# Kernel optimization log

Hardware: AMD Instinct MI355X
Metric: run time of the kernel (lower is better)

Reference implementation:

```python
import jax, jax.numpy as jnp
import numpy as np

N, NF, D, H, L, FFN, E, EF = 2048, 64, 256, 8, 6, 1024, 32768, 16
HD = D // H
MAXDEG, MAXDIST = 64, 8


def setup_inputs() -> dict:
    key = jax.random.key(0)
    ks = jax.random.split(key, 32)
    s = 0.02
    nrm = lambda k, sh: (jax.random.normal(k, sh, jnp.float32) * s)
    return {
        "x": jax.random.normal(ks[0], (N, NF), jnp.float32),
        "edge_attr": jax.random.normal(ks[1], (E, EF), jnp.float32),
        "node_proj_w": nrm(ks[2], (D, NF)),
        "node_proj_b": jnp.zeros((D,), jnp.float32),
        "in_deg_emb": nrm(ks[3], (MAXDEG + 1, D)),
        "out_deg_emb": nrm(ks[4], (MAXDEG + 1, D)),
        "dist_bias": nrm(ks[5], (MAXDIST + 2, H)),
        "edge_proj_w": nrm(ks[6], (H, EF)),
        "edge_proj_b": jnp.zeros((H,), jnp.float32),
        "cls_token": nrm(ks[7], (1, D)),
        "q_w": nrm(ks[8], (L, D, D)), "q_b": jnp.zeros((L, D)),
        "k_w": nrm(ks[9], (L, D, D)), "k_b": jnp.zeros((L, D)),
        "v_w": nrm(ks[10], (L, D, D)), "v_b": jnp.zeros((L, D)),
        "o_w": nrm(ks[11], (L, D, D)), "o_b": jnp.zeros((L, D)),
        "ffn1_w": nrm(ks[12], (L, FFN, D)), "ffn1_b": jnp.zeros((L, FFN)),
        "ffn2_w": nrm(ks[13], (L, D, FFN)), "ffn2_b": jnp.zeros((L, D)),
        "ln1_s": jnp.ones((L, D)), "ln1_b": jnp.zeros((L, D)),
        "ln2_s": jnp.ones((L, D)), "ln2_b": jnp.zeros((L, D)),
        "fn_s": jnp.ones((D,)), "fn_b": jnp.zeros((D,)),
        "edge_index": jax.random.randint(ks[14], (2, E), 0, N, dtype=jnp.int32),
        "dist_matrix": jax.random.randint(ks[15], (N, N), 0, MAXDIST + 2, dtype=jnp.int32),
    }


def _ln(v, s, b):
    m = v.mean(-1, keepdims=True)
    va = v.var(-1, keepdims=True)
    return (v - m) / jnp.sqrt(va + 1e-5) * s + b


def _forward(x, edge_attr, node_proj_w, node_proj_b, in_deg_emb, out_deg_emb,
             dist_bias, edge_proj_w, edge_proj_b, cls_token,
             q_w, q_b, k_w, k_b, v_w, v_b, o_w, o_b,
             ffn1_w, ffn1_b, ffn2_w, ffn2_b,
             ln1_s, ln1_b, ln2_s, ln2_b, fn_s, fn_b,
             edge_index, dist_matrix):
    # node embedding + degree encoding
    h = x @ node_proj_w.T + node_proj_b  # (N, D)
    ones = jnp.ones((E,), jnp.int32)
    in_deg = jnp.clip(jax.ops.segment_sum(ones, edge_index[1], num_segments=N), 0, MAXDEG)
    out_deg = jnp.clip(jax.ops.segment_sum(ones, edge_index[0], num_segments=N), 0, MAXDEG)
    h = h + in_deg_emb[in_deg] + out_deg_emb[out_deg]
    h = jnp.concatenate([cls_token, h], axis=0)  # (N+1, D), CLS at row 0
    Nf = N + 1
    # spatial bias: pad dist matrix with zeros for CLS, then embed
    dist_p = jnp.pad(jnp.clip(dist_matrix, 0, MAXDIST + 1), ((1, 0), (1, 0)))
    bias = dist_bias[dist_p]  # (Nf, Nf, H)
    # edge-feature bias: scatter-add projected edge features into dense (N,N,H)
    proj = edge_attr @ edge_proj_w.T + edge_proj_b  # (E, H)
    ebias = jnp.zeros((N, N, H), h.dtype).at[edge_index[0], edge_index[1]].add(proj)
    bias = bias + jnp.pad(ebias, ((1, 0), (1, 0), (0, 0)))
    bias_t = bias.transpose(2, 0, 1)  # (H, Nf, Nf)
    scale = np.sqrt(HD).astype(np.float32)
    for l in range(L):
        hn = _ln(h, ln1_s[l], ln1_b[l])
        Q = (hn @ q_w[l].T + q_b[l]).reshape(Nf, H, HD).transpose(1, 0, 2)
        K = (hn @ k_w[l].T + k_b[l]).reshape(Nf, H, HD).transpose(1, 0, 2)
        V = (hn @ v_w[l].T + v_b[l]).reshape(Nf, H, HD).transpose(1, 0, 2)
        logits = jnp.einsum('hnd,hmd->hnm', Q, K) / scale + bias_t
        attn = jax.nn.softmax(logits, axis=-1)
        o = jnp.einsum('hnm,hmd->hnd', attn, V).transpose(1, 0, 2).reshape(Nf, D)
        h = h + o @ o_w[l].T + o_b[l]
        hn2 = _ln(h, ln2_s[l], ln2_b[l])
        h = h + jax.nn.gelu(hn2 @ ffn1_w[l].T + ffn1_b[l], approximate=False) @ ffn2_w[l].T + ffn2_b[l]
    h = _ln(h, fn_s, fn_b)
    return h, h[0]


def reference(x, edge_attr, node_proj_w, node_proj_b, in_deg_emb, out_deg_emb,
              dist_bias, edge_proj_w, edge_proj_b, cls_token,
              q_w, q_b, k_w, k_b, v_w, v_b, o_w, o_b,
              ffn1_w, ffn1_b, ffn2_w, ffn2_b,
              ln1_s, ln1_b, ln2_s, ln2_b, fn_s, fn_b,
              edge_index, dist_matrix):
    return _forward(x, edge_attr, node_proj_w, node_proj_b, in_deg_emb, out_deg_emb,
                    dist_bias, edge_proj_w, edge_proj_b, cls_token,
                    q_w, q_b, k_w, k_b, v_w, v_b, o_w, o_b,
                    ffn1_w, ffn1_b, ffn2_w, ffn2_b,
                    ln1_s, ln1_b, ln2_s, ln2_b, fn_s, fn_b,
                    edge_index, dist_matrix)
```

## Files before the change

kernel.cpp:

```cpp
#include <hip/hip_runtime.h>
#include <math.h>

#define N_ 2048
#define NF_IN 64
#define D_ 256
#define H_ 8
#define HD_ 32
#define L_ 6
#define FFN_ 1024
#define E_ 32768
#define EF_ 16
#define NF 2049
#define MAXDEG_ 64
#define BSTRIDE 2112
#define RPAD 2112
#define NSPLIT 4

typedef __attribute__((ext_vector_type(8))) short bf16x8;
typedef __attribute__((ext_vector_type(4))) float f32x4;

__device__ inline unsigned short f2b(float f){
  union { float f; unsigned u; } v; v.f = f;
  unsigned r = (v.u + 0x7fffu + ((v.u >> 16) & 1u)) >> 16;
  return (unsigned short)r;
}
__device__ inline float b2f(short s){
  union { unsigned u; float f; } v; v.u = ((unsigned)(unsigned short)s) << 16;
  return v.f;
}

__device__ inline void atomic_add_bf16(short* p, float add){
  unsigned* wp = (unsigned*)((size_t)p & ~(size_t)3);
  bool hi = ((size_t)p & 2) != 0;
  unsigned old = *wp, assumed;
  do {
    assumed = old;
    unsigned short cur = hi ? (unsigned short)(assumed >> 16)
                            : (unsigned short)(assumed & 0xffffu);
    float f = b2f((short)cur) + add;
    unsigned short nb = f2b(f);
    unsigned nw = hi ? ((assumed & 0x0000ffffu) | ((unsigned)nb << 16))
                     : ((assumed & 0xffff0000u) | (unsigned)nb);
    old = atomicCAS(wp, assumed, nw);
  } while (old != assumed);
}

__device__ inline float wred_sum(float v){
  #pragma unroll
  for (int o = 32; o > 0; o >>= 1) v += __shfl_down(v, o, 64);
  return v;
}

__global__ void zero_int(int* p, int n){
  int i = blockIdx.x * blockDim.x + threadIdx.x;
  if (i < n) p[i] = 0;
}

__global__ void deg_count(const int* __restrict__ ei, int* __restrict__ ind,
                          int* __restrict__ outd){
  int e = blockIdx.x * blockDim.x + threadIdx.x;
  if (e >= E_) return;
  atomicAdd(&outd[ei[e]], 1);
  atomicAdd(&ind[ei[E_ + e]], 1);
}

__global__ void embed_k(const float* __restrict__ x, const float* __restrict__ W,
                        const float* __restrict__ b, const float* __restrict__ inE,
                        const float* __restrict__ outE, const int* __restrict__ ind,
                        const int* __restrict__ outd, const float* __restrict__ cls,
                        float* __restrict__ h){
  int i = blockIdx.x, d = threadIdx.x;
  if (i == 0){ h[d] = cls[d]; return; }
  int n = i - 1;
  const float4* xr = (const float4*)(x + (long)n * NF_IN);
  const float4* wr = (const float4*)(W + (long)d * NF_IN);
  float acc = b[d];
  #pragma unroll
  for (int k = 0; k < NF_IN / 4; k++){
    float4 a = xr[k], w = wr[k];
    acc += a.x * w.x + a.y * w.y + a.z * w.z + a.w * w.w;
  }
  int id = min(ind[n], MAXDEG_), od = min(outd[n], MAXDEG_);
  acc += inE[(long)id * D_ + d] + outE[(long)od * D_ + d];
  h[(long)i * D_ + d] = acc;
}

__global__ void bias_fill(const int* __restrict__ dist, const float* __restrict__ db,
                          short* __restrict__ bb){
  __shared__ float lutS[10][H_];
  int i = blockIdx.x;
  if (threadIdx.x < 80) ((float*)lutS)[threadIdx.x] = db[threadIdx.x];
  __syncthreads();
  for (int u = threadIdx.x; u < BSTRIDE / 8; u += 256){
    int dp[8];
    #pragma unroll
    for (int k = 0; k < 8; k++){
      int j = u * 8 + k;
      int d = 0;
      if (i > 0 && j > 0 && j < NF){
        int dv = dist[(long)(i - 1) * N_ + (j - 1)];
        d = max(0, min(dv, 9));
      }
      dp[k] = (j < NF) ? d : -1;
    }
    #pragma unroll
    for (int h = 0; h < H_; h++){
      short s[8];
      #pragma unroll
      for (int k = 0; k < 8; k++)
        s[k] = (dp[k] >= 0) ? (short)f2b(lutS[dp[k]][h]) : (short)0;
      *(bf16x8*)(bb + ((long)h * NF + i) * BSTRIDE + u * 8) = *(bf16x8*)s;
    }
  }
}

__global__ void edge_bias(const float* __restrict__ ea, const float* __restrict__ W,
                          const float* __restrict__ b, const int* __restrict__ ei,
                          short* __restrict__ bb){
  int e = blockIdx.x * blockDim.x + threadIdx.x;
  if (e >= E_) return;
  float a[EF_];
  #pragma unroll
  for (int k = 0; k < EF_; k++) a[k] = ea[(long)e * EF_ + k];
  int src = ei[e], dst = ei[E_ + e];
  #pragma unroll
  for (int h = 0; h < H_; h++){
    float p = b[h];
    #pragma unroll
    for (int k = 0; k < EF_; k++) p += a[k] * W[h * EF_ + k];
    atomic_add_bf16(bb + ((long)h * NF + src + 1) * BSTRIDE + (dst + 1), p);
  }
}

__global__ void w2b(const float* __restrict__ src, short* __restrict__ dst,
                    long n, long per, long ostride, long ooff){
  long i = (long)blockIdx.x * 256 + threadIdx.x;
  if (i >= n) return;
  long l = i / per, r = i - l * per;
  dst[l * ostride + ooff + r] = (short)f2b(src[i]);
}

__global__ void ln_k(const float* __restrict__ in, const float* __restrict__ s,
                     const float* __restrict__ b, float* __restrict__ outf,
                     short* __restrict__ outb, int dup0){
  __shared__ float r1[4], r2[4];
  int i = blockIdx.x, d = threadIdx.x;
  float v = in[(long)i * D_ + d];
  float s1 = wred_sum(v), s2 = wred_sum(v * v);
  if ((d & 63) == 0){ r1[d >> 6] = s1; r2[d >> 6] = s2; }
  __syncthreads();
  float S1 = r1[0] + r1[1] + r1[2] + r1[3];
  float S2 = r2[0] + r2[1] + r2[2] + r2[3];
  float m = S1 * (1.0f / D_);
  float var = S2 * (1.0f / D_) - m * m;
  float y = (v - m) * rsqrtf(var + 1e-5f) * s[d] + b[d];
  if (outf){
    outf[(long)i * D_ + d] = y;
    if (dup0 && i == 0) outf[(long)NF * D_ + d] = y;
  }
  if (outb) outb[(long)i * D_ + d] = (short)f2b(y);
}

__global__ __launch_bounds__(256) void qkv_gemm(const short* __restrict__ A,
    const short* __restrict__ Wall, const float* __restrict__ qb,
    const float* __restrict__ kb, const float* __restrict__ vb,
    short* __restrict__ QKb, short* __restrict__ Vtg, int l){
  const int z = blockIdx.z;
  const short* W = Wall + ((long)(l * 3 + z)) * D_ * D_;
  const float* bsp = (z == 0) ? qb : (z == 1) ? kb : vb;
  __shared__ __align__(16) short As[64][40], Ws[64][40];
  const int tid = threadIdx.x, lane = tid & 63, wave = tid >> 6;
  const int col = lane & 15, quad = lane >> 4;
  const int wm = wave & 1, wn = wave >> 1;
  const int bm = blockIdx.x * 64, bn = blockIdx.y * 64;
  const f32x4 zero4 = {0.f, 0.f, 0.f, 0.f};
  f32x4 acc[2][2] = {{zero4, zero4}, {zero4, zero4}};
  const int row = tid >> 2, seg = tid & 3;
  for (int k0 = 0; k0 < D_; k0 += 32){
    __syncthreads();
    bf16x8 av = (bf16x8)(short)0;
    int gm = bm + row;
    if (gm < NF) av = *(const bf16x8*)(A + (long)gm * D_ + k0 + seg * 8);
    *(bf16x8*)&As[row][seg * 8] = av;
    *(bf16x8*)&Ws[row][seg * 8] = *(const bf16x8*)(W + (long)(bn + row) * D_ + k0 + seg * 8);
    __syncthreads();
    bf16x8 a0 = *(const bf16x8*)&As[wm * 32 + col][quad * 8];
    bf16x8 a1 = *(const bf16x8*)&As[wm * 32 + 16 + col][quad * 8];
    bf16x8 b0 = *(const bf16x8*)&Ws[wn * 32 + col][quad * 8];
    bf16x8 b1 = *(const bf16x8*)&Ws[wn * 32 + 16 + col][quad * 8];
    acc[0][0] = __builtin_amdgcn_mfma_f32_16x16x32_bf16(a0, b0, acc[0][0], 0, 0, 0);
    acc[0][1] = __builtin_amdgcn_mfma_f32_16x16x32_bf16(a0, b1, acc[0][1], 0, 0, 0);
    acc[1][0] = __builtin_amdgcn_mfma_f32_16x16x32_bf16(a1, b0, acc[1][0], 0, 0, 0);
    acc[1][1] = __builtin_amdgcn_mfma_f32_16x16x32_bf16(a1, b1, acc[1][1], 0, 0, 0);
  }
  #pragma unroll
  for (int i = 0; i < 2; i++)
    #pragma unroll
    for (int j = 0; j < 2; j++)
      #pragma unroll
      for (int r = 0; r < 4; r++){
        int gm = bm + wm * 32 + i * 16 + quad * 4 + r;
        if (gm >= NF) continue;
        int gn = bn + wn * 32 + j * 16 + col;
        float v = acc[i][j][r] + bsp[gn];
        if (z < 2) QKb[(long)z * NF * D_ + (long)gm * D_ + gn] = (short)f2b(v);
        else       Vtg[(long)gn * BSTRIDE + gm] = (short)f2b(v);
      }
}

template<int ACT, int RES, int OUTF, int OUTB, int ATOM>
__global__ __launch_bounds__(256) void mgemm(const short* __restrict__ A,
    const short* __restrict__ W, const float* __restrict__ bs,
    const float* __restrict__ R, float* __restrict__ Cf, short* __restrict__ Cb,
    int M, int Nn, int Kc, int Kstride){
  __shared__ __align__(16) short As[64][40], Ws[64][40];
  const int tid = threadIdx.x, lane = tid & 63, wave = tid >> 6;
  const int col = lane & 15, quad = lane >> 4;
  const int wm = wave & 1, wn = wave >> 1;
  const int bm = blockIdx.x * 64, bn = blockIdx.y * 64;
  const int koff = blockIdx.z * Kc;
  const f32x4 zero4 = {0.f, 0.f, 0.f, 0.f};
  f32x4 acc[2][2] = {{zero4, zero4}, {zero4, zero4}};
  const int row = tid >> 2, seg = tid & 3;
  for (int k0 = 0; k0 < Kc; k0 += 32){
    __syncthreads();
    bf16x8 av = (bf16x8)(short)0;
    int gm = bm + row;
    if (gm < M) av = *(const bf16x8*)(A + (long)gm * Kstride + koff + k0 + seg * 8);
    *(bf16x8*)&As[row][seg * 8] = av;
    *(bf16x8*)&Ws[row][seg * 8] =
      *(const bf16x8*)(W + (long)(bn + row) * Kstride + koff + k0 + seg * 8);
    __syncthreads();
    bf16x8 a0 = *(const bf16x8*)&As[wm * 32 + col][quad * 8];
    bf16x8 a1 = *(const bf16x8*)&As[wm * 32 + 16 + col][quad * 8];
    bf16x8 b0 = *(const bf16x8*)&Ws[wn * 32 + col][quad * 8];
    bf16x8 b1 = *(const bf16x8*)&Ws[wn * 32 + 16 + col][quad * 8];
    acc[0][0] = __builtin_amdgcn_mfma_f32_16x16x32_bf16(a0, b0, acc[0][0], 0, 0, 0);
    acc[0][1] = __builtin_amdgcn_mfma_f32_16x16x32_bf16(a0, b1, acc[0][1], 0, 0, 0);
    acc[1][0] = __builtin_amdgcn_mfma_f32_16x16x32_bf16(a1, b0, acc[1][0], 0, 0, 0);
    acc[1][1] = __builtin_amdgcn_mfma_f32_16x16x32_bf16(a1, b1, acc[1][1], 0, 0, 0);
  }
  #pragma unroll
  for (int i = 0; i < 2; i++)
    #pragma unroll
    for (int j = 0; j < 2; j++)
      #pragma unroll
      for (int r = 0; r < 4; r++){
        int gm = bm + wm * 32 + i * 16 + quad * 4 + r;
        if (gm >= M) continue;
        int gn = bn + wn * 32 + j * 16 + col;
        if (ATOM){
          float v = acc[i][j][r] + (blockIdx.z == 0 ? bs[gn] : 0.f);
          atomicAdd(&Cf[(long)gm * Nn + gn], v);
        } else {
          float v = acc[i][j][r] + bs[gn];
          if (ACT == 1) v = v * 0.5f * (1.0f + erff(v * 0.70710678118654752f));
          if (RES) v += R[(long)gm * Nn + gn];
          if (OUTF) Cf[(long)gm * Nn + gn] = v;
          if (OUTB) Cb[(long)gm * Nn + gn] = (short)f2b(v);
        }
      }
}

__global__ __launch_bounds__(256) void fattn_k(const short* __restrict__ Qb,
    const short* __restrict__ Kb, const short* __restrict__ Vtg,
    const short* __restrict__ biasb, float* __restrict__ Opart,
    float* __restrict__ Lpart){
  __shared__ __align__(16) short Ks[64][40];
  __shared__ __align__(16) short Vt[32][72];
  __shared__ __align__(16) short PB[4][16][72];

  const int tid = threadIdx.x, wave = tid >> 6, lane = tid & 63;
  const int col = lane & 15, quad = lane >> 4;
  const int h = blockIdx.y, qz = blockIdx.z;
  const int i0b = blockIdx.x * 64;
  const int i0 = i0b + wave * 16;
  const int t0 = (qz == 0) ? 0 : 9 + 8 * (qz - 1);
  const int t1 = t0 + ((qz == 0) ? 9 : 8);

  int qrow = min(i0 + col, NF - 1);
  bf16x8 qf = *(const bf16x8*)(Qb + (long)qrow * D_ + h * HD_ + quad * 8);

  f32x4 oacc0 = {0.f, 0.f, 0.f, 0.f}, oacc1 = {0.f, 0.f, 0.f, 0.f};
  float rs[4] = {0.f, 0.f, 0.f, 0.f};
  const f32x4 zero4 = {0.f, 0.f, 0.f, 0.f};
  const float scale = 0.17677669529663687f;

  for (int t = t0; t < t1; t++){
    const int j0 = t * 64;
    __syncthreads();
    {
      int key = tid >> 2, seg = tid & 3;
      int j = j0 + key;
      bf16x8 kv = (bf16x8)(short)0;
      if (j < NF) kv = *(const bf16x8*)(Kb + (long)j * D_ + h * HD_ + seg * 8);
      *(bf16x8*)&Ks[key][seg * 8] = kv;
    }
    {
      int d = tid >> 3, seg = tid & 7;
      *(bf16x8*)&Vt[d][seg * 8] =
        *(const bf16x8*)(Vtg + (long)(h * HD_ + d) * BSTRIDE + j0 + seg * 8);
    }
    #pragma unroll
    for (int it = 0; it < 2; it++){
      int idx = it * 64 + lane;
      int rw = idx >> 3, seg = idx & 7;
      int irow = min(i0b + wave * 16 + rw, NF - 1);
      *(bf16x8*)&PB[wave][rw][seg * 8] =
        *(const bf16x8*)(biasb + ((long)h * NF + irow) * BSTRIDE + j0 + seg * 8);
    }
    __syncthreads();

    f32x4 sacc[4];
    #pragma unroll
    for (int t4 = 0; t4 < 4; t4++){
      bf16x8 kf = *(const bf16x8*)&Ks[t4 * 16 + col][quad * 8];
      sacc[t4] = __builtin_amdgcn_mfma_f32_16x16x32_bf16(qf, kf, zero4, 0, 0, 0);
    }

    const bool tail = (j0 + 64 > NF);
    #pragma unroll
    for (int r = 0; r < 4; r++){
      #pragma unroll
      for (int t4 = 0; t4 < 4; t4++){
        float bv = b2f(PB[wave][quad * 4 + r][t4 * 16 + col]);
        float p = __expf(sacc[t4][r] * scale + bv);
        if (tail && (j0 + t4 * 16 + col >= NF)) p = 0.f;
        rs[r] += p;
        PB[wave][quad * 4 + r][t4 * 16 + col] = (short)f2b(p);
      }
    }

    #pragma unroll
    for (int ks = 0; ks < 2; ks++){
      bf16x8 af = *(const bf16x8*)&PB[wave][col][ks * 32 + quad * 8];
      bf16x8 v0 = *(const bf16x8*)&Vt[col][ks * 32 + quad * 8];
      bf16x8 v1 = *(const bf16x8*)&Vt[16 + col][ks * 32 + quad * 8];
      oacc0 = __builtin_amdgcn_mfma_f32_16x16x32_bf16(af, v0, oacc0, 0, 0, 0);
      oacc1 = __builtin_amdgcn_mfma_f32_16x16x32_bf16(af, v1, oacc1, 0, 0, 0);
    }
  }

  #pragma unroll
  for (int r = 0; r < 4; r++){
    #pragma unroll
    for (int o = 1; o < 16; o <<= 1) rs[r] += __shfl_xor(rs[r], o, 64);
  }
  long pi = ((long)qz * H_ + h) * RPAD + i0 + quad * 4;
  #pragma unroll
  for (int r = 0; r < 4; r++){
    Opart[(pi + r) * HD_ + col] = oacc0[r];
    Opart[(pi + r) * HD_ + 16 + col] = oacc1[r];
    if (col == 0) Lpart[pi + r] = rs[r];
  }
}

__global__ void attn_merge(const float* __restrict__ Op, const float* __restrict__ Lp,
                           short* __restrict__ omb){
  int i = blockIdx.x;
  int h = threadIdx.x >> 5, d = threadIdx.x & 31;
  float s = 0.f, o = 0.f;
  #pragma unroll
  for (int q = 0; q < NSPLIT; q++){
    long pi = ((long)q * H_ + h) * RPAD + i;
    s += Lp[pi];
    o += Op[pi * HD_ + d];
  }
  omb[(long)i * D_ + h * HD_ + d] = (short)f2b(o / s);
}

extern "C" void kernel_launch(void* const* d_in, const int* in_sizes, int n_in,
                              void* d_out, int out_size, void* d_ws, size_t ws_size,
                              hipStream_t stream){
  const float* x    = (const float*)d_in[0];
  const float* ea   = (const float*)d_in[1];
  const float* npw  = (const float*)d_in[2];
  const float* npb  = (const float*)d_in[3];
  const float* inE  = (const float*)d_in[4];
  const float* outE = (const float*)d_in[5];
  const float* db   = (const float*)d_in[6];
  const float* epw  = (const float*)d_in[7];
  const float* epb  = (const float*)d_in[8];
  const float* cls  = (const float*)d_in[9];
  const float* qw   = (const float*)d_in[10];
  const float* qb   = (const float*)d_in[11];
  const float* kw   = (const float*)d_in[12];
  const float* kb   = (const float*)d_in[13];
  const float* vw   = (const float*)d_in[14];
  const float* vb   = (const float*)d_in[15];
  const float* ow   = (const float*)d_in[16];
  const float* ob   = (const float*)d_in[17];
  const float* f1w  = (const float*)d_in[18];
  const float* f1b  = (const float*)d_in[19];
  const float* f2w  = (const float*)d_in[20];
  const float* f2bp = (const float*)d_in[21];
  const float* ln1s = (const float*)d_in[22];
  const float* ln1b = (const float*)d_in[23];
  const float* ln2s = (const float*)d_in[24];
  const float* ln2b = (const float*)d_in[25];
  const float* fns  = (const float*)d_in[26];
  const float* fnb  = (const float*)d_in[27];
  const int*   ei   = (const int*)d_in[28];
  const int*   dist = (const int*)d_in[29];

  float* ws = (float*)d_ws;
  long off = 0;
  float* h     = ws + off; off += (long)NF * D_;
  float* Opart = ws + off; off += (long)NSPLIT * H_ * RPAD * HD_;
  float* Lpart = ws + off; off += (long)NSPLIT * H_ * RPAD;
  short* biasb = (short*)(ws + off); off += ((long)H_ * NF * BSTRIDE + 1) / 2;
  short* hnb   = (short*)(ws + off); off += ((long)NF * D_ + 1) / 2;
  short* QKb   = (short*)(ws + off); off += (long)NF * D_;
  short* Vtg   = (short*)(ws + off); off += ((long)D_ * BSTRIDE + 1) / 2;
  short* omb   = (short*)(ws + off); off += ((long)NF * D_ + 1) / 2;
  short* midb  = (short*)(ws + off); off += ((long)NF * FFN_ + 1) / 2;
  short* wqkv  = (short*)(ws + off); off += ((long)3 * L_ * D_ * D_ + 1) / 2;
  short* owb   = (short*)(ws + off); off += ((long)L_ * D_ * D_ + 1) / 2;
  short* f1wb  = (short*)(ws + off); off += ((long)L_ * FFN_ * D_ + 1) / 2;
  short* f2wb  = (short*)(ws + off); off += ((long)L_ * FFN_ * D_ + 1) / 2;
  int*   ind   = (int*)(ws + off);
  int*   outd  = ind + N_;

  zero_int<<<(2 * N_ + 255) / 256, 256, 0, stream>>>(ind, 2 * N_);
  deg_count<<<(E_ + 255) / 256, 256, 0, stream>>>(ei, ind, outd);
  embed_k<<<NF, D_, 0, stream>>>(x, npw, npb, inE, outE, ind, outd, cls, h);
  bias_fill<<<NF, 256, 0, stream>>>(dist, db, biasb);
  edge_bias<<<(E_ + 255) / 256, 256, 0, stream>>>(ea, epw, epb, ei, biasb);

  {
    long nw = (long)L_ * D_ * D_;
    int gb = (int)((nw + 255) / 256);
    w2b<<<gb, 256, 0, stream>>>(qw, wqkv, nw, (long)D_ * D_, (long)3 * D_ * D_, 0);
    w2b<<<gb, 256, 0, stream>>>(kw, wqkv, nw, (long)D_ * D_, (long)3 * D_ * D_, (long)D_ * D_);
    w2b<<<gb, 256, 0, stream>>>(vw, wqkv, nw, (long)D_ * D_, (long)3 * D_ * D_, (long)2 * D_ * D_);
    w2b<<<gb, 256, 0, stream>>>(ow, owb, nw, nw, 0, 0);
    long nf = (long)L_ * FFN_ * D_;
    int gf = (int)((nf + 255) / 256);
    w2b<<<gf, 256, 0, stream>>>(f1w, f1wb, nf, nf, 0, 0);
    w2b<<<gf, 256, 0, stream>>>(f2w, f2wb, nf, nf, 0, 0);
  }

  dim3 gQKV((NF + 63) / 64, D_ / 64, 3);
  dim3 gO((NF + 63) / 64, D_ / 64, 2);
  dim3 gF((NF + 63) / 64, FFN_ / 64, 1);
  dim3 gF2((NF + 63) / 64, D_ / 64, 4);
  dim3 gA((NF + 63) / 64, H_, NSPLIT);
  for (int l = 0; l < L_; l++){
    ln_k<<<NF, D_, 0, stream>>>(h, ln1s + l * D_, ln1b + l * D_, nullptr, hnb, 0);
    qkv_gemm<<<gQKV, 256, 0, stream>>>(hnb, wqkv, qb + l * D_, kb + l * D_, vb + l * D_,
                                       QKb, Vtg, l);
    fattn_k<<<gA, 256, 0, stream>>>(QKb, QKb + (long)NF * D_, Vtg, biasb, Opart, Lpart);
    attn_merge<<<NF, 256, 0, stream>>>(Opart, Lpart, omb);
    mgemm<0,0,0,0,1><<<gO, 256, 0, stream>>>(omb, owb + (long)l * D_ * D_, ob + l * D_,
                                             nullptr, h, nullptr, NF, D_, 128, D_);
    ln_k<<<NF, D_, 0, stream>>>(h, ln2s + l * D_, ln2b + l * D_, nullptr, hnb, 0);
    mgemm<1,0,0,1,0><<<gF, 256, 0, stream>>>(hnb, f1wb + (long)l * FFN_ * D_, f1b + l * FFN_,
                                             nullptr, nullptr, midb, NF, FFN_, D_, D_);
    mgemm<0,0,0,0,1><<<gF2, 256, 0, stream>>>(midb, f2wb + (long)l * FFN_ * D_, f2bp + l * D_,
                                              nullptr, h, nullptr, NF, D_, 256, FFN_);
  }
  ln_k<<<NF, D_, 0, stream>>>(h, fns, fnb, (float*)d_out, nullptr, 1);
}
```

Before: 695.1 us.

## Store attention bias in fp8, fuse attn merge into out-proj GEMM, batch weight casts

Shrinks the precomputed per-head attention bias tensor from bf16 to fp8 (e4m3), halving the bytes read by the attention kernel each layer, with fp8 atomic CAS for edge bias accumulation. Folds the split-K attention merge (sum of partials divided by the normalizer) into the A-tile load of the output projection GEMM, removing one kernel and its intermediate buffer. Merges six weight-cast launches into one, and keeps softmax probabilities in registers before a single LDS write. The fp8 bias loses precision, and edge contributions accumulated through fp8 atomics compound rounding error.

```diff
diff --git a/kernel.cpp b/kernel.cpp
--- a/kernel.cpp
+++ b/kernel.cpp
@@ -24,23 +24,37 @@
   unsigned r = (v.u + 0x7fffu + ((v.u >> 16) & 1u)) >> 16;
   return (unsigned short)r;
 }
-__device__ inline float b2f(short s){
-  union { unsigned u; float f; } v; v.u = ((unsigned)(unsigned short)s) << 16;
-  return v.f;
-}
-
-__device__ inline void atomic_add_bf16(short* p, float add){
+
+__device__ inline unsigned char f2fp8(float f){
+  unsigned u = __float_as_uint(f);
+  unsigned s = (u >> 24) & 0x80u;
+  float a = fabsf(f);
+  if (a >= 448.f) return (unsigned char)(s | 0x7Eu);
+  if (a < 0.015625f){
+    int k = (int)rintf(a * 512.f);
+    return (unsigned char)(s | (unsigned)k);
+  }
+  int e; float m = frexpf(a, &e);
+  int E = e - 1;
+  int m3 = (int)rintf(m * 16.f) - 8;
+  if (m3 == 8){ E++; m3 = 0; }
+  if (E > 8){ E = 8; m3 = 6; }
+  if (E == 8 && m3 > 6) m3 = 6;
+  return (unsigned char)(s | (unsigned)((E + 7) << 3) | (unsigned)m3);
+}
+__device__ inline float fp82f(unsigned char b){
+  return __builtin_amdgcn_cvt_f32_fp8((int)b, 0);
+}
+
+__device__ inline void atomic_add_fp8(unsigned char* p, float add){
   unsigned* wp = (unsigned*)((size_t)p & ~(size_t)3);
-  bool hi = ((size_t)p & 2) != 0;
+  int sh = (int)((size_t)p & 3) * 8;
   unsigned old = *wp, assumed;
   do {
     assumed = old;
-    unsigned short cur = hi ? (unsigned short)(assumed >> 16)
-                            : (unsigned short)(assumed & 0xffffu);
-    float f = b2f((short)cur) + add;
-    unsigned short nb = f2b(f);
-    unsigned nw = hi ? ((assumed & 0x0000ffffu) | ((unsigned)nb << 16))
-                     : ((assumed & 0xffff0000u) | (unsigned)nb);
+    unsigned char cur = (unsigned char)((assumed >> sh) & 0xFFu);
+    float f = fp82f(cur) + add;
+    unsigned nw = (assumed & ~(0xFFu << sh)) | ((unsigned)f2fp8(f) << sh);
     old = atomicCAS(wp, assumed, nw);
   } while (old != assumed);
 }
@@ -86,10 +100,10 @@
 }
 
 __global__ void bias_fill(const int* __restrict__ dist, const float* __restrict__ db,
-                          short* __restrict__ bb){
-  __shared__ float lutS[10][H_];
+                          unsigned char* __restrict__ bb){
+  __shared__ unsigned char lut8[10][H_];
   int i = blockIdx.x;
-  if (threadIdx.x < 80) ((float*)lutS)[threadIdx.x] = db[threadIdx.x];
+  if (threadIdx.x < 80) ((unsigned char*)lut8)[threadIdx.x] = f2fp8(db[threadIdx.x]);
   __syncthreads();
   for (int u = threadIdx.x; u < BSTRIDE / 8; u += 256){
     int dp[8];
@@ -105,18 +119,22 @@
     }
     #pragma unroll
     for (int h = 0; h < H_; h++){
-      short s[8];
+      unsigned lo = 0, hi = 0;
       #pragma unroll
-      for (int k = 0; k < 8; k++)
-        s[k] = (dp[k] >= 0) ? (short)f2b(lutS[dp[k]][h]) : (short)0;
-      *(bf16x8*)(bb + ((long)h * NF + i) * BSTRIDE + u * 8) = *(bf16x8*)s;
+      for (int k = 0; k < 4; k++){
+        unsigned b0 = (dp[k] >= 0) ? lut8[dp[k]][h] : 0u;
+        unsigned b1 = (dp[4 + k] >= 0) ? lut8[dp[4 + k]][h] : 0u;
+        lo |= b0 << (8 * k);
+        hi |= b1 << (8 * k);
+      }
+      *(uint2*)(bb + ((long)h * NF + i) * BSTRIDE + u * 8) = make_uint2(lo, hi);
     }
   }
 }
 
 __global__ void edge_bias(const float* __restrict__ ea, const float* __restrict__ W,
                           const float* __restrict__ b, const int* __restrict__ ei,
-                          short* __restrict__ bb){
+                          unsigned char* __restrict__ bb){
   int e = blockIdx.x * blockDim.x + threadIdx.x;
   if (e >= E_) return;
   float a[EF_];
@@ -128,16 +146,28 @@
     float p = b[h];
     #pragma unroll
     for (int k = 0; k < EF_; k++) p += a[k] * W[h * EF_ + k];
-    atomic_add_bf16(bb + ((long)h * NF + src + 1) * BSTRIDE + (dst + 1), p);
-  }
-}
-
-__global__ void w2b(const float* __restrict__ src, short* __restrict__ dst,
-                    long n, long per, long ostride, long ooff){
+    atomic_add_fp8(bb + ((long)h * NF + src + 1) * BSTRIDE + (dst + 1), p);
+  }
+}
+
+__global__ void w2b_all(const float* __restrict__ qw, const float* __restrict__ kw,
+                        const float* __restrict__ vw, const float* __restrict__ ow,
+                        const float* __restrict__ f1w, const float* __restrict__ f2w,
+                        short* __restrict__ wqkv, short* __restrict__ owb,
+                        short* __restrict__ f1wb, short* __restrict__ f2wb){
   long i = (long)blockIdx.x * 256 + threadIdx.x;
-  if (i >= n) return;
-  long l = i / per, r = i - l * per;
-  dst[l * ostride + ooff + r] = (short)f2b(src[i]);
+  const long DD = (long)D_ * D_, LDD = (long)L_ * DD, LFD = (long)L_ * FFN_ * D_;
+  if (i < LDD){
+    long l = i / DD, r = i - l * DD;
+    wqkv[l * 3 * DD + r]          = (short)f2b(qw[i]);
+    wqkv[l * 3 * DD + DD + r]     = (short)f2b(kw[i]);
+    wqkv[l * 3 * DD + 2 * DD + r] = (short)f2b(vw[i]);
+    owb[i] = (short)f2b(ow[i]);
+  }
+  if (i < LFD){
+    f1wb[i] = (short)f2b(f1w[i]);
+    f2wb[i] = (short)f2b(f2w[i]);
+  }
 }
 
 __global__ void ln_k(const float* __restrict__ in, const float* __restrict__ s,
@@ -208,10 +238,11 @@
       }
 }
 
-template<int ACT, int RES, int OUTF, int OUTB, int ATOM>
+template<int ACT, int ATOM, int MERGE>
 __global__ __launch_bounds__(256) void mgemm(const short* __restrict__ A,
+    const float* __restrict__ Op, const float* __restrict__ Lp,
     const short* __restrict__ W, const float* __restrict__ bs,
-    const float* __restrict__ R, float* __restrict__ Cf, short* __restrict__ Cb,
+    float* __restrict__ Cf, short* __restrict__ Cb,
     int M, int Nn, int Kc, int Kstride){
   __shared__ __align__(16) short As[64][40], Ws[64][40];
   const int tid = threadIdx.x, lane = tid & 63, wave = tid >> 6;
@@ -224,10 +255,34 @@
   const int row = tid >> 2, seg = tid & 3;
   for (int k0 = 0; k0 < Kc; k0 += 32){
     __syncthreads();
-    bf16x8 av = (bf16x8)(short)0;
     int gm = bm + row;
-    if (gm < M) av = *(const bf16x8*)(A + (long)gm * Kstride + koff + k0 + seg * 8);
-    *(bf16x8*)&As[row][seg * 8] = av;
+    if (MERGE){
+      int kg = koff + k0 + seg * 8;
+      int hh = kg >> 5, d0 = kg & 31;
+      short sarr[8] = {0,0,0,0,0,0,0,0};
+      if (gm < M){
+        float o0=0,o1=0,o2=0,o3=0,o4=0,o5=0,o6=0,o7=0, sl=0.f;
+        #pragma unroll
+        for (int q = 0; q < NSPLIT; q++){
+          long rb = (long)(q * H_ + hh) * RPAD + gm;
+          const float* op = Op + rb * HD_ + d0;
+          float4 v0 = *(const float4*)op, v1 = *(const float4*)(op + 4);
+          o0 += v0.x; o1 += v0.y; o2 += v0.z; o3 += v0.w;
+          o4 += v1.x; o5 += v1.y; o6 += v1.z; o7 += v1.w;
+          sl += Lp[rb];
+        }
+        float inv = 1.0f / sl;
+        sarr[0]=(short)f2b(o0*inv); sarr[1]=(short)f2b(o1*inv);
+        sarr[2]=(short)f2b(o2*inv); sarr[3]=(short)f2b(o3*inv);
+        sarr[4]=(short)f2b(o4*inv); sarr[5]=(short)f2b(o5*inv);
+        sarr[6]=(short)f2b(o6*inv); sarr[7]=(short)f2b(o7*inv);
+      }
+      *(bf16x8*)&As[row][seg * 8] = *(bf16x8*)sarr;
+    } else {
+      bf16x8 av = (bf16x8)(short)0;
+      if (gm < M) av = *(const bf16x8*)(A + (long)gm * Kstride + koff + k0 + seg * 8);
+      *(bf16x8*)&As[row][seg * 8] = av;
+    }
     *(bf16x8*)&Ws[row][seg * 8] =
       *(const bf16x8*)(W + (long)(bn + row) * Kstride + koff + k0 + seg * 8);
     __syncthreads();
@@ -255,26 +310,23 @@
         } else {
           float v = acc[i][j][r] + bs[gn];
           if (ACT == 1) v = v * 0.5f * (1.0f + erff(v * 0.70710678118654752f));
-          if (RES) v += R[(long)gm * Nn + gn];
-          if (OUTF) Cf[(long)gm * Nn + gn] = v;
-          if (OUTB) Cb[(long)gm * Nn + gn] = (short)f2b(v);
+          Cb[(long)gm * Nn + gn] = (short)f2b(v);
         }
       }
 }
 
 __global__ __launch_bounds__(256) void fattn_k(const short* __restrict__ Qb,
     const short* __restrict__ Kb, const short* __restrict__ Vtg,
-    const short* __restrict__ biasb, float* __restrict__ Opart,
+    const unsigned char* __restrict__ bias8, float* __restrict__ Opart,
     float* __restrict__ Lpart){
   __shared__ __align__(16) short Ks[64][40];
   __shared__ __align__(16) short Vt[32][72];
-  __shared__ __align__(16) short PB[4][16][72];
+  __shared__ __align__(16) unsigned char PS[4][2304];
 
   const int tid = threadIdx.x, wave = tid >> 6, lane = tid & 63;
   const int col = lane & 15, quad = lane >> 4;
   const int h = blockIdx.y, qz = blockIdx.z;
-  const int i0b = blockIdx.x * 64;
-  const int i0 = i0b + wave * 16;
+  const int i0 = blockIdx.x * 64 + wave * 16;
   const int t0 = (qz == 0) ? 0 : 9 + 8 * (qz - 1);
   const int t1 = t0 + ((qz == 0) ? 9 : 8);
 
@@ -285,6 +337,7 @@
   float rs[4] = {0.f, 0.f, 0.f, 0.f};
   const f32x4 zero4 = {0.f, 0.f, 0.f, 0.f};
   const float scale = 0.17677669529663687f;
+  short* Pp = (short*)PS[wave];
 
   for (int t = t0; t < t1; t++){
     const int j0 = t * 64;
@@ -301,13 +354,13 @@
       *(bf16x8*)&Vt[d][seg * 8] =
         *(const bf16x8*)(Vtg + (long)(h * HD_ + d) * BSTRIDE + j0 + seg * 8);
     }
-    #pragma unroll
-    for (int it = 0; it < 2; it++){
-      int idx = it * 64 + lane;
-      int rw = idx >> 3, seg = idx & 7;
-      int irow = min(i0b + wave * 16 + rw, NF - 1);
-      *(bf16x8*)&PB[wave][rw][seg * 8] =
-        *(const bf16x8*)(biasb + ((long)h * NF + irow) * BSTRIDE + j0 + seg * 8);
+    {
+      int rw = lane >> 2, seg = lane & 3;
+      int irow = min(i0 + rw, NF - 1);
+      uint4 bv = *(const uint4*)(bias8 + (long)(h * NF + irow) * BSTRIDE + j0 + seg * 16);
+      uint2* d2 = (uint2*)&PS[wave][rw * 80 + seg * 16];
+      d2[0] = make_uint2(bv.x, bv.y);
+      d2[1] = make_uint2(bv.z, bv.w);
     }
     __syncthreads();
 
@@ -323,17 +376,22 @@
     for (int r = 0; r < 4; r++){
       #pragma unroll
       for (int t4 = 0; t4 < 4; t4++){
-        float bv = b2f(PB[wave][quad * 4 + r][t4 * 16 + col]);
+        float bv = fp82f(PS[wave][(quad * 4 + r) * 80 + t4 * 16 + col]);
         float p = __expf(sacc[t4][r] * scale + bv);
         if (tail && (j0 + t4 * 16 + col >= NF)) p = 0.f;
         rs[r] += p;
-        PB[wave][quad * 4 + r][t4 * 16 + col] = (short)f2b(p);
+        sacc[t4][r] = p;
       }
     }
+    #pragma unroll
+    for (int r = 0; r < 4; r++)
+      #pragma unroll
+      for (int t4 = 0; t4 < 4; t4++)
+        Pp[(quad * 4 + r) * 72 + t4 * 16 + col] = (short)f2b(sacc[t4][r]);
 
     #pragma unroll
     for (int ks = 0; ks < 2; ks++){
-      bf16x8 af = *(const bf16x8*)&PB[wave][col][ks * 32 + quad * 8];
+      bf16x8 af = *(const bf16x8*)&Pp[col * 72 + ks * 32 + quad * 8];
       bf16x8 v0 = *(const bf16x8*)&Vt[col][ks * 32 + quad * 8];
       bf16x8 v1 = *(const bf16x8*)&Vt[16 + col][ks * 32 + quad * 8];
       oacc0 = __builtin_amdgcn_mfma_f32_16x16x32_bf16(af, v0, oacc0, 0, 0, 0);
@@ -353,20 +411,6 @@
     Opart[(pi + r) * HD_ + 16 + col] = oacc1[r];
     if (col == 0) Lpart[pi + r] = rs[r];
   }
-}
-
-__global__ void attn_merge(const float* __restrict__ Op, const float* __restrict__ Lp,
-                           short* __restrict__ omb){
-  int i = blockIdx.x;
-  int h = threadIdx.x >> 5, d = threadIdx.x & 31;
-  float s = 0.f, o = 0.f;
-  #pragma unroll
-  for (int q = 0; q < NSPLIT; q++){
-    long pi = ((long)q * H_ + h) * RPAD + i;
-    s += Lp[pi];
-    o += Op[pi * HD_ + d];
-  }
-  omb[(long)i * D_ + h * HD_ + d] = (short)f2b(o / s);
 }
 
 extern "C" void kernel_launch(void* const* d_in, const int* in_sizes, int n_in,
@@ -408,11 +452,11 @@
   float* h     = ws + off; off += (long)NF * D_;
   float* Opart = ws + off; off += (long)NSPLIT * H_ * RPAD * HD_;
   float* Lpart = ws + off; off += (long)NSPLIT * H_ * RPAD;
-  short* biasb = (short*)(ws + off); off += ((long)H_ * NF * BSTRIDE + 1) / 2;
+  unsigned char* bias8 = (unsigned char*)(ws + off);
+  off += ((long)H_ * NF * BSTRIDE + 3) / 4;
   short* hnb   = (short*)(ws + off); off += ((long)NF * D_ + 1) / 2;
   short* QKb   = (short*)(ws + off); off += (long)NF * D_;
   short* Vtg   = (short*)(ws + off); off += ((long)D_ * BSTRIDE + 1) / 2;
-  short* omb   = (short*)(ws + off); off += ((long)NF * D_ + 1) / 2;
   short* midb  = (short*)(ws + off); off += ((long)NF * FFN_ + 1) / 2;
   short* wqkv  = (short*)(ws + off); off += ((long)3 * L_ * D_ * D_ + 1) / 2;
   short* owb   = (short*)(ws + off); off += ((long)L_ * D_ * D_ + 1) / 2;
@@ -424,20 +468,12 @@
   zero_int<<<(2 * N_ + 255) / 256, 256, 0, stream>>>(ind, 2 * N_);
   deg_count<<<(E_ + 255) / 256, 256, 0, stream>>>(ei, ind, outd);
   embed_k<<<NF, D_, 0, stream>>>(x, npw, npb, inE, outE, ind, outd, cls, h);
-  bias_fill<<<NF, 256, 0, stream>>>(dist, db, biasb);
-  edge_bias<<<(E_ + 255) / 256, 256, 0, stream>>>(ea, epw, epb, ei, biasb);
-
+  bias_fill<<<NF, 256, 0, stream>>>(dist, db, bias8);
+  edge_bias<<<(E_ + 255) / 256, 256, 0, stream>>>(ea, epw, epb, ei, bias8);
   {
-    long nw = (long)L_ * D_ * D_;
-    int gb = (int)((nw + 255) / 256);
-    w2b<<<gb, 256, 0, stream>>>(qw, wqkv, nw, (long)D_ * D_, (long)3 * D_ * D_, 0);
-    w2b<<<gb, 256, 0, stream>>>(kw, wqkv, nw, (long)D_ * D_, (long)3 * D_ * D_, (long)D_ * D_);
-    w2b<<<gb, 256, 0, stream>>>(vw, wqkv, nw, (long)D_ * D_, (long)3 * D_ * D_, (long)2 * D_ * D_);
-    w2b<<<gb, 256, 0, stream>>>(ow, owb, nw, nw, 0, 0);
-    long nf = (long)L_ * FFN_ * D_;
-    int gf = (int)((nf + 255) / 256);
-    w2b<<<gf, 256, 0, stream>>>(f1w, f1wb, nf, nf, 0, 0);
-    w2b<<<gf, 256, 0, stream>>>(f2w, f2wb, nf, nf, 0, 0);
+    long LFD = (long)L_ * FFN_ * D_;
+    w2b_all<<<(int)((LFD + 255) / 256), 256, 0, stream>>>(qw, kw, vw, ow, f1w, f2w,
+                                                          wqkv, owb, f1wb, f2wb);
   }
 
   dim3 gQKV((NF + 63) / 64, D_ / 64, 3);
@@ -449,15 +485,17 @@
     ln_k<<<NF, D_, 0, stream>>>(h, ln1s + l * D_, ln1b + l * D_, nullptr, hnb, 0);
     qkv_gemm<<<gQKV, 256, 0, stream>>>(hnb, wqkv, qb + l * D_, kb + l * D_, vb + l * D_,
                                        QKb, Vtg, l);
-    fattn_k<<<gA, 256, 0, stream>>>(QKb, QKb + (long)NF * D_, Vtg, biasb, Opart, Lpart);
-    attn_merge<<<NF, 256, 0, stream>>>(Opart, Lpart, omb);
-    mgemm<0,0,0,0,1><<<gO, 256, 0, stream>>>(omb, owb + (long)l * D_ * D_, ob + l * D_,
-                                             nullptr, h, nullptr, NF, D_, 128, D_);
+    fattn_k<<<gA, 256, 0, stream>>>(QKb, QKb + (long)NF * D_, Vtg, bias8, Opart, Lpart);
+    mgemm<0,1,1><<<gO, 256, 0, stream>>>(nullptr, Opart, Lpart,
+                                         owb + (long)l * D_ * D_, ob + l * D_,
+                                         h, nullptr, NF, D_, 128, D_);
     ln_k<<<NF, D_, 0, stream>>>(h, ln2s + l * D_, ln2b + l * D_, nullptr, hnb, 0);
-    mgemm<1,0,0,1,0><<<gF, 256, 0, stream>>>(hnb, f1wb + (long)l * FFN_ * D_, f1b + l * FFN_,
-                                             nullptr, nullptr, midb, NF, FFN_, D_, D_);
-    mgemm<0,0,0,0,1><<<gF2, 256, 0, stream>>>(midb, f2wb + (long)l * FFN_ * D_, f2bp + l * D_,
-                                              nullptr, h, nullptr, NF, D_, 256, FFN_);
+    mgemm<1,0,0><<<gF, 256, 0, stream>>>(hnb, nullptr, nullptr,
+                                         f1wb + (long)l * FFN_ * D_, f1b + l * FFN_,
+                                         nullptr, midb, NF, FFN_, D_, D_);
+    mgemm<0,1,0><<<gF2, 256, 0, stream>>>(midb, nullptr, nullptr,
+                                          f2wb + (long)l * FFN_ * D_, f2bp + l * D_,
+                                          h, nullptr, NF, D_, 256, FFN_);
   }
   ln_k<<<NF, D_, 0, stream>>>(h, fns, fnb, (float*)d_out, nullptr, 1);
 }
```

Result: no change. 686.1 us (-1.3%).
